# Performance work log

Measured on AMD Instinct MI355X. Metric: run time of the kernel, lower is better.

The kernel has to match this reference:

```python
import jax, jax.numpy as jnp
import numpy as np

N, E, H, ED = 100000, 1600000, 128, 64
BN_EPS = 1e-5


def setup_inputs() -> dict:
    key = jax.random.key(0)
    ks = jax.random.split(key, 8)
    s = 1.0 / np.sqrt(H)
    return {
        "h": jax.random.normal(ks[0], (N, H), jnp.float32),
        "ei": jax.random.randint(ks[1], (2, E), 0, N, jnp.int64),
        "ea": jax.random.normal(ks[2], (E, ED), jnp.float32),
        "valid_f": jnp.ones((N, 1), jnp.float32),
        "W_edge": jax.random.normal(ks[3], (ED, H), jnp.float32) / np.sqrt(ED),
        "b_edge": jnp.zeros((H,), jnp.float32),
        "W1": jax.random.normal(ks[4], (H, H), jnp.float32) * s,
        "b1": jnp.zeros((H,), jnp.float32),
        "W2": jax.random.normal(ks[5], (H, H), jnp.float32) * s,
        "b2": jnp.zeros((H,), jnp.float32),
        "eps_gine": jnp.zeros((1,), jnp.float32),
        "bn_gamma": jnp.ones((H,), jnp.float32),
        "bn_beta": jnp.zeros((H,), jnp.float32),
    }


def reference(h, ei, ea, valid_f, W_edge, b_edge, W1, b1, W2, b2, eps_gine, bn_gamma, bn_beta):
    src, dst = ei[0], ei[1]  # message flows j(src) -> i(dst)
    # GINE message: relu(x_j + lin(edge_attr))
    msg = jax.nn.relu(h[src] + ea @ W_edge + b_edge)          # [E, H]
    agg = jax.ops.segment_sum(msg, dst, num_segments=N)       # [N, H]
    # GIN update: mlp((1 + eps) * x_i + aggr)
    z = (1.0 + eps_gine[0]) * h + agg
    z = jax.nn.relu(z @ W1 + b1) @ W2 + b2                    # 2-layer MLP
    z = jax.nn.relu(z)
    # BatchNorm over nodes (training-mode batch stats, biased var)
    mean = jnp.mean(z, axis=0)
    var = jnp.var(z, axis=0)
    h_new = (z - mean) * jax.lax.rsqrt(var + BN_EPS) * bn_gamma + bn_beta
    # dropout p=0.0 -> identity; residual + valid mask
    return (h + h_new) * valid_f
```

## Files before the change

### kernel.cpp

```cpp
#include <hip/hip_runtime.h>

#define H 128
#define ED 64
#define CH 16
#define SCB 256
#define SCT 256

typedef __attribute__((ext_vector_type(8))) short short8;
typedef __attribute__((ext_vector_type(4))) float f32x4;
typedef __attribute__((ext_vector_type(4))) unsigned int u32x4;

__device__ __align__(16) float g_stats[256];

__device__ __forceinline__ unsigned short f2bf(float f) {
    unsigned u = __float_as_uint(f);
    unsigned r = u + 0x7fffu + ((u >> 16) & 1u);
    return (unsigned short)(r >> 16);
}
__device__ __forceinline__ float bf2f(unsigned short h) {
    return __uint_as_float(((unsigned)h) << 16);
}
__device__ __forceinline__ float4 ntld4(const float* p) {
    f32x4 v = __builtin_nontemporal_load((const f32x4*)p);
    return make_float4(v[0], v[1], v[2], v[3]);
}
__device__ __forceinline__ uint4 ntldu4(const unsigned* p) {
    u32x4 v = __builtin_nontemporal_load((const u32x4*)p);
    return make_uint4(v[0], v[1], v[2], v[3]);
}

__global__ void k_zero_stats() {
    if (threadIdx.x < 256) g_stats[threadIdx.x] = 0.f;
}

__global__ void k_hist(const int* __restrict__ ei, int* __restrict__ cnt, int E) {
    if (blockIdx.x == 0 && threadIdx.x < 256) g_stats[threadIdx.x] = 0.f;
    for (int e = blockIdx.x * blockDim.x + threadIdx.x; e < E;
         e += gridDim.x * blockDim.x)
        atomicAdd(&cnt[ei[E + e]], 1);
}

__global__ __launch_bounds__(SCT) void k_scanA(const int* __restrict__ cnt,
                                               int* __restrict__ bsum, int N) {
    __shared__ int part[SCT];
    const int b = blockIdx.x, t = threadIdx.x;
    const int chunk = (N + SCB - 1) / SCB;
    const int tch = (chunk + SCT - 1) / SCT;
    const int lo = b * chunk + t * tch;
    const int hi = min(lo + tch, min((b + 1) * chunk, N));
    int s = 0;
    for (int i = lo; i < hi; ++i) s += (cnt[i] + 15) >> 4;
    part[t] = s;
    __syncthreads();
    for (int d = SCT / 2; d > 0; d >>= 1) {
        if (t < d) part[t] += part[t + d];
        __syncthreads();
    }
    if (t == 0) bsum[b] = part[0];
}

__global__ __launch_bounds__(SCB) void k_scanB(const int* __restrict__ bsum,
                                               int* __restrict__ bpre,
                                               int* __restrict__ toffN) {
    __shared__ int part[SCB];
    const int t = threadIdx.x;
    int v = bsum[t];
    part[t] = v;
    __syncthreads();
    for (int d = 1; d < SCB; d <<= 1) {
        int x = (t >= d) ? part[t - d] : 0;
        __syncthreads();
        part[t] += x;
        __syncthreads();
    }
    bpre[t] = part[t] - v;
    if (t == SCB - 1) *toffN = part[t];
}

__global__ __launch_bounds__(SCT) void k_scanC(const int* __restrict__ cnt,
                                               const int* __restrict__ bpre,
                                               int* __restrict__ toff,
                                               int* __restrict__ tileDst, int N) {
    __shared__ int part[SCT];
    const int b = blockIdx.x, t = threadIdx.x;
    const int chunk = (N + SCB - 1) / SCB;
    const int tch = (chunk + SCT - 1) / SCT;
    const int lo = b * chunk + t * tch;
    const int hi = min(lo + tch, min((b + 1) * chunk, N));
    int ls = 0;
    for (int i = lo; i < hi; ++i) ls += (cnt[i] + 15) >> 4;
    part[t] = ls;
    __syncthreads();
    for (int d = 1; d < SCT; d <<= 1) {
        int x = (t >= d) ? part[t - d] : 0;
        __syncthreads();
        part[t] += x;
        __syncthreads();
    }
    int run = bpre[b] + part[t] - ls;
    for (int i = lo; i < hi; ++i) {
        toff[i] = run;
        int c = (cnt[i] + 15) >> 4;
        for (int j = 0; j < c; ++j) tileDst[run + j] = i;
        run += c;
    }
}

__global__ void k_fillp(const int* __restrict__ ei, const int* __restrict__ toff,
                        int* __restrict__ cur, int* __restrict__ tilePerm, int E) {
    for (int e = blockIdx.x * blockDim.x + threadIdx.x; e < E;
         e += gridDim.x * blockDim.x) {
        int d = ei[E + e];
        int pos = atomicAdd(&cur[d], 1);
        int tile = toff[d] + (pos >> 4);
        tilePerm[(tile << 4) + (pos & 15)] = e;
    }
}

__global__ __launch_bounds__(256, 3) void k_edge_t(
    const float* __restrict__ hN, const int* __restrict__ ei,
    const float* __restrict__ ea, const float* __restrict__ We,
    const float* __restrict__ be, const int* __restrict__ toff,
    const int* __restrict__ tileDst, const int* __restrict__ tilePerm,
    float* __restrict__ agg, int N, int E)
{
    __shared__ __align__(16) short sBf[8][2][64][8];
    const int tid = threadIdx.x;
    for (int idx = tid; idx < 8 * 2 * 64; idx += 256) {
        int t = idx >> 7, s = (idx >> 6) & 1, ll = idx & 63;
        int ra = ll & 15, kgg = ll >> 4;
        short8 f;
#pragma unroll
        for (int b = 0; b < 8; ++b) {
            int k = (s << 5) + (kgg << 3) + b;
            f[b] = (short)f2bf(We[k * H + (t << 4) + ra]);
        }
        *(short8*)&sBf[t][s][ll][0] = f;
    }
    const int l = tid & 63, w = tid >> 6;
    const int rA = l & 15, kg = l >> 4;
    float beT[8];
#pragma unroll
    for (int t = 0; t < 8; ++t) beT[t] = be[(t << 4) + rA];
    __syncthreads();

    const int nT = toff[N];
    const int gw = (blockIdx.x << 2) | w;
    const int nW = gridDim.x << 2;
    if (gw >= nT) return;

    int peC, srcC, dstC;
    float4 ea0, ea1, ea2, ea3;
    int peN;
    {
        peC = tilePerm[(gw << 4) + rA];
        dstC = tileDst[gw];
        srcC = (peC >= 0) ? ei[peC] : -1;
        const float* ar = ea + (size_t)max(peC, 0) * ED + (kg << 3);
        ea0 = ntld4(ar);      ea1 = ntld4(ar + 4);
        ea2 = ntld4(ar + 32); ea3 = ntld4(ar + 36);
        peN = (gw + nW < nT) ? tilePerm[((gw + nW) << 4) + rA] : -1;
    }

    for (int tt = gw; tt < nT; tt += nW) {
        const int s0 = __shfl(srcC, (kg << 2) + 0);
        const int s1 = __shfl(srcC, (kg << 2) + 1);
        const int s2 = __shfl(srcC, (kg << 2) + 2);
        const int s3 = __shfl(srcC, (kg << 2) + 3);
        float hv0[8], hv1[8], hv2[8], hv3[8];
        {
            const float* hp0 = hN + (size_t)max(s0, 0) * H + rA;
            const float* hp1 = hN + (size_t)max(s1, 0) * H + rA;
            const float* hp2 = hN + (size_t)max(s2, 0) * H + rA;
            const float* hp3 = hN + (size_t)max(s3, 0) * H + rA;
#pragma unroll
            for (int t = 0; t < 8; ++t) {
                hv0[t] = hp0[t << 4]; hv1[t] = hp1[t << 4];
                hv2[t] = hp2[t << 4]; hv3[t] = hp3[t << 4];
            }
        }
        const int ttN = tt + nW;
        int srcN = -1, dstN = 0;
        float4 eb0, eb1, eb2, eb3;
        eb0 = eb1 = eb2 = eb3 = make_float4(0.f, 0.f, 0.f, 0.f);
        if (ttN < nT) {
            srcN = (peN >= 0) ? ei[peN] : -1;
            dstN = tileDst[ttN];
            const float* ar = ea + (size_t)max(peN, 0) * ED + (kg << 3);
            eb0 = ntld4(ar);      eb1 = ntld4(ar + 4);
            eb2 = ntld4(ar + 32); eb3 = ntld4(ar + 36);
        }
        const int ttF = tt + 2 * nW;
        const int peF = (ttF < nT) ? tilePerm[(ttF << 4) + rA] : -1;

        short8 A0, A1;
        A0[0] = f2bf(ea0.x); A0[1] = f2bf(ea0.y); A0[2] = f2bf(ea0.z); A0[3] = f2bf(ea0.w);
        A0[4] = f2bf(ea1.x); A0[5] = f2bf(ea1.y); A0[6] = f2bf(ea1.z); A0[7] = f2bf(ea1.w);
        A1[0] = f2bf(ea2.x); A1[1] = f2bf(ea2.y); A1[2] = f2bf(ea2.z); A1[3] = f2bf(ea2.w);
        A1[4] = f2bf(ea3.x); A1[5] = f2bf(ea3.y); A1[6] = f2bf(ea3.z); A1[7] = f2bf(ea3.w);
        f32x4 C[8];
#pragma unroll
        for (int t = 0; t < 8; ++t) {
            short8 b0 = *(const short8*)&sBf[t][0][l][0];
            short8 b1 = *(const short8*)&sBf[t][1][l][0];
            f32x4 c = __builtin_amdgcn_mfma_f32_16x16x32_bf16(
                A0, b0, (f32x4){0.f, 0.f, 0.f, 0.f}, 0, 0, 0);
            C[t] = __builtin_amdgcn_mfma_f32_16x16x32_bf16(A1, b1, c, 0, 0, 0);
        }

        const float ok0 = (s0 >= 0) ? 1.f : 0.f;
        const float ok1 = (s1 >= 0) ? 1.f : 0.f;
        const float ok2 = (s2 >= 0) ? 1.f : 0.f;
        const float ok3 = (s3 >= 0) ? 1.f : 0.f;
        float pacc[8];
#pragma unroll
        for (int t = 0; t < 8; ++t) {
            float v = fmaxf(C[t][0] + hv0[t] + beT[t], 0.f) * ok0
                    + fmaxf(C[t][1] + hv1[t] + beT[t], 0.f) * ok1
                    + fmaxf(C[t][2] + hv2[t] + beT[t], 0.f) * ok2
                    + fmaxf(C[t][3] + hv3[t] + beT[t], 0.f) * ok3;
            v += __shfl_xor(v, 16);
            v += __shfl_xor(v, 32);
            pacc[t] = v;
        }
        float vlo = (kg == 0) ? pacc[0] : (kg == 1) ? pacc[1] : (kg == 2) ? pacc[2] : pacc[3];
        float vhi = (kg == 0) ? pacc[4] : (kg == 1) ? pacc[5] : (kg == 2) ? pacc[6] : pacc[7];
        float* qp = agg + (size_t)dstC * H + l;
        atomicAdd(qp, vlo);
        atomicAdd(qp + 64, vhi);

        peC = peN; srcC = srcN; dstC = dstN;
        ea0 = eb0; ea1 = eb1; ea2 = eb2; ea3 = eb3;
        peN = peF;
    }
}

__global__ __launch_bounds__(256, 2) void k_mlp1(
    const float* __restrict__ hN, float* zb, const float* __restrict__ W1,
    const float* __restrict__ b1, const float* __restrict__ epsp, int N)
{
    __shared__ __align__(16) short sBf[8][4][64][8];
    const int tid = threadIdx.x;
    for (int idx = tid; idx < 8 * 4 * 64; idx += 256) {
        int t = idx >> 8, s = (idx >> 6) & 3, ll = idx & 63;
        int ra = ll & 15, kgg = ll >> 4;
        short8 f;
#pragma unroll
        for (int b = 0; b < 8; ++b) {
            int k = (s << 5) + (kgg << 3) + b;
            f[b] = (short)f2bf(W1[k * H + (t << 4) + ra]);
        }
        *(short8*)&sBf[t][s][ll][0] = f;
    }
    __syncthreads();
    const int l = tid & 63, w = tid >> 6;
    const int rA = l & 15, kg = l >> 4;
    const float e1 = 1.f + epsp[0];
    float bT[8];
#pragma unroll
    for (int t = 0; t < 8; ++t) bT[t] = b1[(t << 4) + rA];

    const int nT = (N + CH - 1) / CH;
    for (int tt = blockIdx.x * 4 + w; tt < nT; tt += gridDim.x * 4) {
        const int n0 = tt << 4;
        const int row = min(n0 + rA, N - 1);
        const float* hrow = hN + (size_t)row * H;
        const float* arow = (const float*)zb + (size_t)row * H;
        f32x4 C[8];
#pragma unroll
        for (int t = 0; t < 8; ++t) C[t] = (f32x4){0.f, 0.f, 0.f, 0.f};

        const float* hp = hrow + (kg << 3);
        const float* ap = arow + (kg << 3);
        float4 h0 = ntld4(hp), h1 = ntld4(hp + 4);
        float4 g0 = ntld4(ap), g1 = ntld4(ap + 4);
#pragma unroll
        for (int s = 0; s < 4; ++s) {
            float4 h0n, h1n, g0n, g1n;
            if (s < 3) {
                const float* hp2 = hrow + ((s + 1) << 5) + (kg << 3);
                const float* ap2 = arow + ((s + 1) << 5) + (kg << 3);
                h0n = ntld4(hp2); h1n = ntld4(hp2 + 4);
                g0n = ntld4(ap2); g1n = ntld4(ap2 + 4);
            }
            float z[8];
            z[0] = fmaf(e1, h0.x, g0.x); z[1] = fmaf(e1, h0.y, g0.y);
            z[2] = fmaf(e1, h0.z, g0.z); z[3] = fmaf(e1, h0.w, g0.w);
            z[4] = fmaf(e1, h1.x, g1.x); z[5] = fmaf(e1, h1.y, g1.y);
            z[6] = fmaf(e1, h1.z, g1.z); z[7] = fmaf(e1, h1.w, g1.w);
            short8 ah, al;
#pragma unroll
            for (int j = 0; j < 8; ++j) {
                unsigned short hi = f2bf(z[j]);
                ah[j] = (short)hi;
                al[j] = (short)f2bf(z[j] - bf2f(hi));
            }
#pragma unroll
            for (int t = 0; t < 8; ++t) {
                short8 B = *(const short8*)&sBf[t][s][l][0];
                C[t] = __builtin_amdgcn_mfma_f32_16x16x32_bf16(ah, B, C[t], 0, 0, 0);
                C[t] = __builtin_amdgcn_mfma_f32_16x16x32_bf16(al, B, C[t], 0, 0, 0);
            }
            if (s < 3) { h0 = h0n; h1 = h1n; g0 = g0n; g1 = g1n; }
        }
#pragma unroll
        for (int t = 0; t < 8; ++t) {
#pragma unroll
            for (int rg = 0; rg < 4; ++rg) {
                int n = n0 + (kg << 2) + rg;
                float y = fmaxf(C[t][rg] + bT[t], 0.f);
                unsigned short hi = f2bf(y);
                unsigned short lo = f2bf(y - bf2f(hi));
                if (n < N)
                    ((unsigned*)zb)[(size_t)n * H + (t << 4) + rA] =
                        ((unsigned)hi << 16) | (unsigned)lo;
            }
        }
    }
}

__global__ __launch_bounds__(256, 2) void k_mlp2(
    float* zb, const float* __restrict__ W2, const float* __restrict__ b2, int N)
{
    __shared__ __align__(16) short sBf[8][4][64][8];
    const int tid = threadIdx.x;
    for (int idx = tid; idx < 8 * 4 * 64; idx += 256) {
        int t = idx >> 8, s = (idx >> 6) & 3, ll = idx & 63;
        int ra = ll & 15, kgg = ll >> 4;
        short8 f;
#pragma unroll
        for (int b = 0; b < 8; ++b) {
            int k = (s << 5) + (kgg << 3) + b;
            f[b] = (short)f2bf(W2[k * H + (t << 4) + ra]);
        }
        *(short8*)&sBf[t][s][ll][0] = f;
    }
    __syncthreads();
    const int l = tid & 63, w = tid >> 6;
    const int rA = l & 15, kg = l >> 4;
    float bT[8];
#pragma unroll
    for (int t = 0; t < 8; ++t) bT[t] = b2[(t << 4) + rA];
    float ps[8], pq[8];
#pragma unroll
    for (int t = 0; t < 8; ++t) { ps[t] = 0.f; pq[t] = 0.f; }

    const int nT = (N + CH - 1) / CH;
    for (int tt = blockIdx.x * 4 + w; tt < nT; tt += gridDim.x * 4) {
        const int n0 = tt << 4;
        const int row = min(n0 + rA, N - 1);
        const unsigned* yrow = (const unsigned*)zb + (size_t)row * H;
        f32x4 C[8];
#pragma unroll
        for (int t = 0; t < 8; ++t) C[t] = (f32x4){0.f, 0.f, 0.f, 0.f};

        const unsigned* yp = yrow + (kg << 3);
        uint4 u0 = ntldu4(yp), u1 = ntldu4(yp + 4);
#pragma unroll
        for (int s = 0; s < 4; ++s) {
            uint4 u0n, u1n;
            if (s < 3) {
                const unsigned* yp2 = yrow + ((s + 1) << 5) + (kg << 3);
                u0n = ntldu4(yp2); u1n = ntldu4(yp2 + 4);
            }
            short8 ah, al;
            ah[0] = (short)(u0.x >> 16); al[0] = (short)(u0.x & 0xffffu);
            ah[1] = (short)(u0.y >> 16); al[1] = (short)(u0.y & 0xffffu);
            ah[2] = (short)(u0.z >> 16); al[2] = (short)(u0.z & 0xffffu);
            ah[3] = (short)(u0.w >> 16); al[3] = (short)(u0.w & 0xffffu);
            ah[4] = (short)(u1.x >> 16); al[4] = (short)(u1.x & 0xffffu);
            ah[5] = (short)(u1.y >> 16); al[5] = (short)(u1.y & 0xffffu);
            ah[6] = (short)(u1.z >> 16); al[6] = (short)(u1.z & 0xffffu);
            ah[7] = (short)(u1.w >> 16); al[7] = (short)(u1.w & 0xffffu);
#pragma unroll
            for (int t = 0; t < 8; ++t) {
                short8 B = *(const short8*)&sBf[t][s][l][0];
                C[t] = __builtin_amdgcn_mfma_f32_16x16x32_bf16(ah, B, C[t], 0, 0, 0);
                C[t] = __builtin_amdgcn_mfma_f32_16x16x32_bf16(al, B, C[t], 0, 0, 0);
            }
            if (s < 3) { u0 = u0n; u1 = u1n; }
        }
#pragma unroll
        for (int t = 0; t < 8; ++t) {
#pragma unroll
            for (int rg = 0; rg < 4; ++rg) {
                int n = n0 + (kg << 2) + rg;
                float z2 = fmaxf(C[t][rg] + bT[t], 0.f);
                bool v = (n < N);
                if (v) ((float*)zb)[(size_t)n * H + (t << 4) + rA] = z2;
                float zc = v ? z2 : 0.f;
                ps[t] += zc;
                pq[t] += zc * zc;
            }
        }
    }
#pragma unroll
    for (int t = 0; t < 8; ++t) {
        float a = ps[t]; a += __shfl_xor(a, 16); a += __shfl_xor(a, 32); ps[t] = a;
        float b = pq[t]; b += __shfl_xor(b, 16); b += __shfl_xor(b, 32); pq[t] = b;
    }
    if (l < 16) {
#pragma unroll
        for (int t = 0; t < 8; ++t) {
            atomicAdd(&g_stats[(t << 4) + l], ps[t]);
            atomicAdd(&g_stats[128 + (t << 4) + l], pq[t]);
        }
    }
}

__global__ void k_final(const float* __restrict__ hN, const float* __restrict__ valid,
                        const float* __restrict__ gamma, const float* __restrict__ beta,
                        float invN, float* __restrict__ out, int N)
{
    __shared__ float sSc[H], sSh[H];
    if (threadIdx.x < H) {
        int t = threadIdx.x;
        float mean = g_stats[t] * invN;
        float var  = g_stats[H + t] * invN - mean * mean;
        float sc = gamma[t] * rsqrtf(var + 1e-5f);
        sSc[t] = sc;
        sSh[t] = beta[t] - mean * sc;
    }
    __syncthreads();
    const int total = N * (H / 4);
    for (int i = blockIdx.x * blockDim.x + threadIdx.x; i < total;
         i += gridDim.x * blockDim.x) {
        int col4 = i & 31;
        int n = i >> 5;
        float4 z = ((float4*)out)[i];
        float4 hv = ntld4(hN + (size_t)i * 4);
        float4 sc = *(const float4*)&sSc[col4 * 4];
        float4 sh = *(const float4*)&sSh[col4 * 4];
        float vf = valid[n];
        float4 r;
        r.x = (hv.x + fmaf(z.x, sc.x, sh.x)) * vf;
        r.y = (hv.y + fmaf(z.y, sc.y, sh.y)) * vf;
        r.z = (hv.z + fmaf(z.z, sc.z, sh.z)) * vf;
        r.w = (hv.w + fmaf(z.w, sc.w, sh.w)) * vf;
        ((float4*)out)[i] = r;
    }
}

__global__ __launch_bounds__(512, 4) void k_edge_a(
    const float* __restrict__ hN, const int* __restrict__ ei,
    const float* __restrict__ ea, const float* __restrict__ We,
    const float* __restrict__ be, float* __restrict__ agg, int E)
{
    __shared__ __align__(16) short sBf[8][2][64][8];
    const int tid = threadIdx.x;
    for (int idx = tid; idx < 8 * 2 * 64; idx += 512) {
        int t = idx >> 7, s = (idx >> 6) & 1, ll = idx & 63;
        int ra = ll & 15, kgg = ll >> 4;
        short8 f;
#pragma unroll
        for (int b = 0; b < 8; ++b) {
            int k = (s << 5) + (kgg << 3) + b;
            f[b] = (short)f2bf(We[k * H + (t << 4) + ra]);
        }
        *(short8*)&sBf[t][s][ll][0] = f;
    }
    const int l = tid & 63, w = tid >> 6;
    const int rA = l & 15, kg = l >> 4;
    float beT[8];
#pragma unroll
    for (int t = 0; t < 8; ++t) beT[t] = be[(t << 4) + rA];
    __syncthreads();

    const int nT = (E + CH - 1) / CH;
    for (int tt = (blockIdx.x << 3) | w; tt < nT; tt += gridDim.x << 3) {
        int e0 = tt * CH;
        const float* ar = ea + (size_t)min(e0 + rA, E - 1) * ED + (kg << 3);
        float4 a0 = *(const float4*)ar,        a1 = *(const float4*)(ar + 4);
        float4 a2 = *(const float4*)(ar + 32), a3 = *(const float4*)(ar + 36);
        int r0 = min(e0 + (kg << 2) + 0, E - 1), r1 = min(e0 + (kg << 2) + 1, E - 1);
        int r2 = min(e0 + (kg << 2) + 2, E - 1), r3 = min(e0 + (kg << 2) + 3, E - 1);
        int s0 = ei[r0], s1 = ei[r1], s2 = ei[r2], s3 = ei[r3];
        int d0 = ei[E + r0], d1 = ei[E + r1], d2 = ei[E + r2], d3 = ei[E + r3];
        float hv0[8], hv1[8], hv2[8], hv3[8];
        const float* hp0 = hN + (size_t)s0 * H + rA;
        const float* hp1 = hN + (size_t)s1 * H + rA;
        const float* hp2 = hN + (size_t)s2 * H + rA;
        const float* hp3 = hN + (size_t)s3 * H + rA;
#pragma unroll
        for (int t = 0; t < 8; ++t) {
            hv0[t] = hp0[t << 4]; hv1[t] = hp1[t << 4];
            hv2[t] = hp2[t << 4]; hv3[t] = hp3[t << 4];
        }
        short8 A0, A1;
        A0[0] = f2bf(a0.x); A0[1] = f2bf(a0.y); A0[2] = f2bf(a0.z); A0[3] = f2bf(a0.w);
        A0[4] = f2bf(a1.x); A0[5] = f2bf(a1.y); A0[6] = f2bf(a1.z); A0[7] = f2bf(a1.w);
        A1[0] = f2bf(a2.x); A1[1] = f2bf(a2.y); A1[2] = f2bf(a2.z); A1[3] = f2bf(a2.w);
        A1[4] = f2bf(a3.x); A1[5] = f2bf(a3.y); A1[6] = f2bf(a3.z); A1[7] = f2bf(a3.w);
        f32x4 C[8];
#pragma unroll
        for (int t = 0; t < 8; ++t) {
            short8 b0 = *(const short8*)&sBf[t][0][l][0];
            short8 b1 = *(const short8*)&sBf[t][1][l][0];
            f32x4 c = __builtin_amdgcn_mfma_f32_16x16x32_bf16(
                A0, b0, (f32x4){0.f, 0.f, 0.f, 0.f}, 0, 0, 0);
            C[t] = __builtin_amdgcn_mfma_f32_16x16x32_bf16(A1, b1, c, 0, 0, 0);
        }
        const int m = E - e0;
        const int r = kg << 2;
        const bool ok0 = (r + 0) < m, ok1 = (r + 1) < m;
        const bool ok2 = (r + 2) < m, ok3 = (r + 3) < m;
        float* q0 = agg + (size_t)d0 * H + rA;
        float* q1 = agg + (size_t)d1 * H + rA;
        float* q2 = agg + (size_t)d2 * H + rA;
        float* q3 = agg + (size_t)d3 * H + rA;
#pragma unroll
        for (int t = 0; t < 8; ++t) {
            if (ok0) atomicAdd(q0 + (t << 4), fmaxf(C[t][0] + hv0[t] + beT[t], 0.f));
            if (ok1) atomicAdd(q1 + (t << 4), fmaxf(C[t][1] + hv1[t] + beT[t], 0.f));
            if (ok2) atomicAdd(q2 + (t << 4), fmaxf(C[t][2] + hv2[t] + beT[t], 0.f));
            if (ok3) atomicAdd(q3 + (t << 4), fmaxf(C[t][3] + hv3[t] + beT[t], 0.f));
        }
    }
}

extern "C" void kernel_launch(void* const* d_in, const int* in_sizes, int n_in,
                              void* d_out, int out_size, void* d_ws, size_t ws_size,
                              hipStream_t stream) {
    const float* hN    = (const float*)d_in[0];
    const int*   ei    = (const int*)d_in[1];
    const float* ea    = (const float*)d_in[2];
    const float* valid = (const float*)d_in[3];
    const float* We    = (const float*)d_in[4];
    const float* be    = (const float*)d_in[5];
    const float* W1    = (const float*)d_in[6];
    const float* b1    = (const float*)d_in[7];
    const float* W2    = (const float*)d_in[8];
    const float* b2    = (const float*)d_in[9];
    const float* epsg  = (const float*)d_in[10];
    const float* gamma = (const float*)d_in[11];
    const float* beta  = (const float*)d_in[12];
    float* out = (float*)d_out;

    const int N = in_sizes[0] / H;
    const int E = in_sizes[1] / 2;

    const int Tcap = (E + 15) / 16 + N;
    const size_t need = ((size_t)3 * N + 1 + 2 * SCB + (size_t)17 * Tcap) * sizeof(int);

    (void)hipMemsetAsync(d_out, 0, (size_t)out_size * sizeof(float), stream);

    if (ws_size >= need) {
        int* cnt      = (int*)d_ws;
        int* cur      = cnt + N;
        int* toff     = cur + N;
        int* bsum     = toff + N + 1;
        int* bpre     = bsum + SCB;
        int* tileDst  = bpre + SCB;
        int* tilePerm = tileDst + Tcap;

        (void)hipMemsetAsync(cnt, 0, (size_t)2 * N * sizeof(int), stream);
        (void)hipMemsetAsync(tilePerm, 0xFF, (size_t)16 * Tcap * sizeof(int), stream);
        k_hist<<<2048, 256, 0, stream>>>(ei, cnt, E);
        k_scanA<<<SCB, SCT, 0, stream>>>(cnt, bsum, N);
        k_scanB<<<1, SCB, 0, stream>>>(bsum, bpre, toff + N);
        k_scanC<<<SCB, SCT, 0, stream>>>(cnt, bpre, toff, tileDst, N);
        k_fillp<<<2048, 256, 0, stream>>>(ei, toff, cur, tilePerm, E);
        k_edge_t<<<2048, 256, 0, stream>>>(hN, ei, ea, We, be, toff, tileDst,
                                           tilePerm, out, N, E);
    } else {
        k_zero_stats<<<1, 256, 0, stream>>>();
        k_edge_a<<<1024, 512, 0, stream>>>(hN, ei, ea, We, be, out, E);
    }

    k_mlp1<<<512, 256, 0, stream>>>(hN, out, W1, b1, epsg, N);
    k_mlp2<<<512, 256, 0, stream>>>(out, W2, b2, N);
    k_final<<<2048, 256, 0, stream>>>(hN, valid, gamma, beta, 1.0f / (float)N,
                                      out, N);
}
```

Measured before the change: 606.9 us.

## Replace three-pass tile scan with atomic tile allocation and fuse MLP layers

Replaces the three scan kernels with a single kernel that hands out tile ranges per destination node using a global atomic counter, and pads only the last tile of each node instead of memsetting the whole tilePerm buffer. The two MLP kernels are fused into one: the first layer's split-bf16 output is staged in per-wave LDS instead of round-tripping through global memory, and both weight matrices are held in shared memory. This removes kernel launches, a large memset and the intermediate global traffic. In exchange, tile order becomes nondeterministic, which loses destination locality, and the larger LDS footprint and 512-thread blocks may reduce occupancy.

```diff
diff --git a/kernel.cpp b/kernel.cpp
--- a/kernel.cpp
+++ b/kernel.cpp
@@ -3,8 +3,6 @@
 #define H 128
 #define ED 64
 #define CH 16
-#define SCB 256
-#define SCT 256
 
 typedef __attribute__((ext_vector_type(8))) short short8;
 typedef __attribute__((ext_vector_type(4))) float f32x4;
@@ -23,10 +21,6 @@
 __device__ __forceinline__ float4 ntld4(const float* p) {
     f32x4 v = __builtin_nontemporal_load((const f32x4*)p);
     return make_float4(v[0], v[1], v[2], v[3]);
-}
-__device__ __forceinline__ uint4 ntldu4(const unsigned* p) {
-    u32x4 v = __builtin_nontemporal_load((const u32x4*)p);
-    return make_uint4(v[0], v[1], v[2], v[3]);
 }
 
 __global__ void k_zero_stats() {
@@ -40,69 +34,22 @@
         atomicAdd(&cnt[ei[E + e]], 1);
 }
 
-__global__ __launch_bounds__(SCT) void k_scanA(const int* __restrict__ cnt,
-                                               int* __restrict__ bsum, int N) {
-    __shared__ int part[SCT];
-    const int b = blockIdx.x, t = threadIdx.x;
-    const int chunk = (N + SCB - 1) / SCB;
-    const int tch = (chunk + SCT - 1) / SCT;
-    const int lo = b * chunk + t * tch;
-    const int hi = min(lo + tch, min((b + 1) * chunk, N));
-    int s = 0;
-    for (int i = lo; i < hi; ++i) s += (cnt[i] + 15) >> 4;
-    part[t] = s;
-    __syncthreads();
-    for (int d = SCT / 2; d > 0; d >>= 1) {
-        if (t < d) part[t] += part[t + d];
-        __syncthreads();
-    }
-    if (t == 0) bsum[b] = part[0];
-}
-
-__global__ __launch_bounds__(SCB) void k_scanB(const int* __restrict__ bsum,
-                                               int* __restrict__ bpre,
-                                               int* __restrict__ toffN) {
-    __shared__ int part[SCB];
-    const int t = threadIdx.x;
-    int v = bsum[t];
-    part[t] = v;
-    __syncthreads();
-    for (int d = 1; d < SCB; d <<= 1) {
-        int x = (t >= d) ? part[t - d] : 0;
-        __syncthreads();
-        part[t] += x;
-        __syncthreads();
-    }
-    bpre[t] = part[t] - v;
-    if (t == SCB - 1) *toffN = part[t];
-}
-
-__global__ __launch_bounds__(SCT) void k_scanC(const int* __restrict__ cnt,
-                                               const int* __restrict__ bpre,
-                                               int* __restrict__ toff,
-                                               int* __restrict__ tileDst, int N) {
-    __shared__ int part[SCT];
-    const int b = blockIdx.x, t = threadIdx.x;
-    const int chunk = (N + SCB - 1) / SCB;
-    const int tch = (chunk + SCT - 1) / SCT;
-    const int lo = b * chunk + t * tch;
-    const int hi = min(lo + tch, min((b + 1) * chunk, N));
-    int ls = 0;
-    for (int i = lo; i < hi; ++i) ls += (cnt[i] + 15) >> 4;
-    part[t] = ls;
-    __syncthreads();
-    for (int d = 1; d < SCT; d <<= 1) {
-        int x = (t >= d) ? part[t - d] : 0;
-        __syncthreads();
-        part[t] += x;
-        __syncthreads();
-    }
-    int run = bpre[b] + part[t] - ls;
-    for (int i = lo; i < hi; ++i) {
-        toff[i] = run;
-        int c = (cnt[i] + 15) >> 4;
-        for (int j = 0; j < c; ++j) tileDst[run + j] = i;
-        run += c;
+__global__ void k_tiles(const int* __restrict__ cnt, int* __restrict__ toff,
+                        int* __restrict__ tileDst, int* __restrict__ tilePerm,
+                        int* __restrict__ tcnt, int N) {
+    for (int d = blockIdx.x * blockDim.x + threadIdx.x; d < N;
+         d += gridDim.x * blockDim.x) {
+        int c = cnt[d];
+        int nt = (c + 15) >> 4;
+        if (nt == 0) continue;
+        int base = atomicAdd(tcnt, nt);
+        toff[d] = base;
+        for (int j = 0; j < nt; ++j) tileDst[base + j] = d;
+        int pad = c & 15;
+        if (pad) {
+            int* lastp = tilePerm + ((size_t)(base + nt - 1) << 4);
+            for (int j = pad; j < 16; ++j) lastp[j] = -1;
+        }
     }
 }
 
@@ -113,14 +60,14 @@
         int d = ei[E + e];
         int pos = atomicAdd(&cur[d], 1);
         int tile = toff[d] + (pos >> 4);
-        tilePerm[(tile << 4) + (pos & 15)] = e;
+        tilePerm[((size_t)tile << 4) + (pos & 15)] = e;
     }
 }
 
 __global__ __launch_bounds__(256, 3) void k_edge_t(
     const float* __restrict__ hN, const int* __restrict__ ei,
     const float* __restrict__ ea, const float* __restrict__ We,
-    const float* __restrict__ be, const int* __restrict__ toff,
+    const float* __restrict__ be, const int* __restrict__ tcnt,
     const int* __restrict__ tileDst, const int* __restrict__ tilePerm,
     float* __restrict__ agg, int N, int E)
 {
@@ -144,7 +91,7 @@
     for (int t = 0; t < 8; ++t) beT[t] = be[(t << 4) + rA];
     __syncthreads();
 
-    const int nT = toff[N];
+    const int nT = tcnt[0];
     const int gw = (blockIdx.x << 2) | w;
     const int nW = gridDim.x << 2;
     if (gw >= nT) return;
@@ -153,13 +100,13 @@
     float4 ea0, ea1, ea2, ea3;
     int peN;
     {
-        peC = tilePerm[(gw << 4) + rA];
+        peC = tilePerm[((size_t)gw << 4) + rA];
         dstC = tileDst[gw];
         srcC = (peC >= 0) ? ei[peC] : -1;
         const float* ar = ea + (size_t)max(peC, 0) * ED + (kg << 3);
         ea0 = ntld4(ar);      ea1 = ntld4(ar + 4);
         ea2 = ntld4(ar + 32); ea3 = ntld4(ar + 36);
-        peN = (gw + nW < nT) ? tilePerm[((gw + nW) << 4) + rA] : -1;
+        peN = (gw + nW < nT) ? tilePerm[((size_t)(gw + nW) << 4) + rA] : -1;
     }
 
     for (int tt = gw; tt < nT; tt += nW) {
@@ -191,7 +138,7 @@
             eb2 = ntld4(ar + 32); eb3 = ntld4(ar + 36);
         }
         const int ttF = tt + 2 * nW;
-        const int peF = (ttF < nT) ? tilePerm[(ttF << 4) + rA] : -1;
+        const int peF = (ttF < nT) ? tilePerm[((size_t)ttF << 4) + rA] : -1;
 
         short8 A0, A1;
         A0[0] = f2bf(ea0.x); A0[1] = f2bf(ea0.y); A0[2] = f2bf(ea0.z); A0[3] = f2bf(ea0.w);
@@ -235,33 +182,45 @@
     }
 }
 
-__global__ __launch_bounds__(256, 2) void k_mlp1(
-    const float* __restrict__ hN, float* zb, const float* __restrict__ W1,
-    const float* __restrict__ b1, const float* __restrict__ epsp, int N)
+__global__ __launch_bounds__(512, 2) void k_mlp(
+    const float* __restrict__ hN, float* zb,
+    const float* __restrict__ W1, const float* __restrict__ b1,
+    const float* __restrict__ W2, const float* __restrict__ b2,
+    const float* __restrict__ epsp, int N)
 {
-    __shared__ __align__(16) short sBf[8][4][64][8];
+    __shared__ __align__(16) short sB1[8][4][64][8];
+    __shared__ __align__(16) short sB2[8][4][64][8];
+    __shared__ __align__(16) unsigned sY[8][16][132];
     const int tid = threadIdx.x;
-    for (int idx = tid; idx < 8 * 4 * 64; idx += 256) {
+    for (int idx = tid; idx < 8 * 4 * 64; idx += 512) {
         int t = idx >> 8, s = (idx >> 6) & 3, ll = idx & 63;
         int ra = ll & 15, kgg = ll >> 4;
-        short8 f;
+        short8 f1, f2;
 #pragma unroll
         for (int b = 0; b < 8; ++b) {
             int k = (s << 5) + (kgg << 3) + b;
-            f[b] = (short)f2bf(W1[k * H + (t << 4) + ra]);
-        }
-        *(short8*)&sBf[t][s][ll][0] = f;
+            f1[b] = (short)f2bf(W1[k * H + (t << 4) + ra]);
+            f2[b] = (short)f2bf(W2[k * H + (t << 4) + ra]);
+        }
+        *(short8*)&sB1[t][s][ll][0] = f1;
+        *(short8*)&sB2[t][s][ll][0] = f2;
     }
     __syncthreads();
     const int l = tid & 63, w = tid >> 6;
     const int rA = l & 15, kg = l >> 4;
     const float e1 = 1.f + epsp[0];
-    float bT[8];
-#pragma unroll
-    for (int t = 0; t < 8; ++t) bT[t] = b1[(t << 4) + rA];
+    float bT1[8], bT2[8];
+#pragma unroll
+    for (int t = 0; t < 8; ++t) {
+        bT1[t] = b1[(t << 4) + rA];
+        bT2[t] = b2[(t << 4) + rA];
+    }
+    float ps[8], pq[8];
+#pragma unroll
+    for (int t = 0; t < 8; ++t) { ps[t] = 0.f; pq[t] = 0.f; }
 
     const int nT = (N + CH - 1) / CH;
-    for (int tt = blockIdx.x * 4 + w; tt < nT; tt += gridDim.x * 4) {
+    for (int tt = blockIdx.x * 8 + w; tt < nT; tt += gridDim.x * 8) {
         const int n0 = tt << 4;
         const int row = min(n0 + rA, N - 1);
         const float* hrow = hN + (size_t)row * H;
@@ -270,19 +229,12 @@
 #pragma unroll
         for (int t = 0; t < 8; ++t) C[t] = (f32x4){0.f, 0.f, 0.f, 0.f};
 
-        const float* hp = hrow + (kg << 3);
-        const float* ap = arow + (kg << 3);
-        float4 h0 = ntld4(hp), h1 = ntld4(hp + 4);
-        float4 g0 = ntld4(ap), g1 = ntld4(ap + 4);
 #pragma unroll
         for (int s = 0; s < 4; ++s) {
-            float4 h0n, h1n, g0n, g1n;
-            if (s < 3) {
-                const float* hp2 = hrow + ((s + 1) << 5) + (kg << 3);
-                const float* ap2 = arow + ((s + 1) << 5) + (kg << 3);
-                h0n = ntld4(hp2); h1n = ntld4(hp2 + 4);
-                g0n = ntld4(ap2); g1n = ntld4(ap2 + 4);
-            }
+            const float* hp = hrow + (s << 5) + (kg << 3);
+            const float* ap = arow + (s << 5) + (kg << 3);
+            float4 h0 = ntld4(hp), h1 = ntld4(hp + 4);
+            float4 g0 = ntld4(ap), g1 = ntld4(ap + 4);
             float z[8];
             z[0] = fmaf(e1, h0.x, g0.x); z[1] = fmaf(e1, h0.y, g0.y);
             z[2] = fmaf(e1, h0.z, g0.z); z[3] = fmaf(e1, h0.w, g0.w);
@@ -297,72 +249,31 @@
             }
 #pragma unroll
             for (int t = 0; t < 8; ++t) {
-                short8 B = *(const short8*)&sBf[t][s][l][0];
+                short8 B = *(const short8*)&sB1[t][s][l][0];
                 C[t] = __builtin_amdgcn_mfma_f32_16x16x32_bf16(ah, B, C[t], 0, 0, 0);
                 C[t] = __builtin_amdgcn_mfma_f32_16x16x32_bf16(al, B, C[t], 0, 0, 0);
             }
-            if (s < 3) { h0 = h0n; h1 = h1n; g0 = g0n; g1 = g1n; }
         }
 #pragma unroll
         for (int t = 0; t < 8; ++t) {
 #pragma unroll
             for (int rg = 0; rg < 4; ++rg) {
-                int n = n0 + (kg << 2) + rg;
-                float y = fmaxf(C[t][rg] + bT[t], 0.f);
+                float y = fmaxf(C[t][rg] + bT1[t], 0.f);
                 unsigned short hi = f2bf(y);
                 unsigned short lo = f2bf(y - bf2f(hi));
-                if (n < N)
-                    ((unsigned*)zb)[(size_t)n * H + (t << 4) + rA] =
-                        ((unsigned)hi << 16) | (unsigned)lo;
-            }
-        }
-    }
-}
-
-__global__ __launch_bounds__(256, 2) void k_mlp2(
-    float* zb, const float* __restrict__ W2, const float* __restrict__ b2, int N)
-{
-    __shared__ __align__(16) short sBf[8][4][64][8];
-    const int tid = threadIdx.x;
-    for (int idx = tid; idx < 8 * 4 * 64; idx += 256) {
-        int t = idx >> 8, s = (idx >> 6) & 3, ll = idx & 63;
-        int ra = ll & 15, kgg = ll >> 4;
-        short8 f;
-#pragma unroll
-        for (int b = 0; b < 8; ++b) {
-            int k = (s << 5) + (kgg << 3) + b;
-            f[b] = (short)f2bf(W2[k * H + (t << 4) + ra]);
-        }
-        *(short8*)&sBf[t][s][ll][0] = f;
-    }
-    __syncthreads();
-    const int l = tid & 63, w = tid >> 6;
-    const int rA = l & 15, kg = l >> 4;
-    float bT[8];
-#pragma unroll
-    for (int t = 0; t < 8; ++t) bT[t] = b2[(t << 4) + rA];
-    float ps[8], pq[8];
-#pragma unroll
-    for (int t = 0; t < 8; ++t) { ps[t] = 0.f; pq[t] = 0.f; }
-
-    const int nT = (N + CH - 1) / CH;
-    for (int tt = blockIdx.x * 4 + w; tt < nT; tt += gridDim.x * 4) {
-        const int n0 = tt << 4;
-        const int row = min(n0 + rA, N - 1);
-        const unsigned* yrow = (const unsigned*)zb + (size_t)row * H;
-        f32x4 C[8];
+                sY[w][(kg << 2) + rg][(t << 4) + rA] =
+                    ((unsigned)hi << 16) | (unsigned)lo;
+            }
+        }
+        __builtin_amdgcn_wave_barrier();
+
 #pragma unroll
         for (int t = 0; t < 8; ++t) C[t] = (f32x4){0.f, 0.f, 0.f, 0.f};
-
-        const unsigned* yp = yrow + (kg << 3);
-        uint4 u0 = ntldu4(yp), u1 = ntldu4(yp + 4);
 #pragma unroll
         for (int s = 0; s < 4; ++s) {
-            uint4 u0n, u1n;
-            if (s < 3) {
-                const unsigned* yp2 = yrow + ((s + 1) << 5) + (kg << 3);
-                u0n = ntldu4(yp2); u1n = ntldu4(yp2 + 4);
-            }
+            const unsigned* yp = &sY[w][rA][(s << 5) + (kg << 3)];
+            uint4 u0 = *(const uint4*)yp;
+            uint4 u1 = *(const uint4*)(yp + 4);
             short8 ah, al;
             ah[0] = (short)(u0.x >> 16); al[0] = (short)(u0.x & 0xffffu);
             ah[1] = (short)(u0.y >> 16); al[1] = (short)(u0.y & 0xffffu);
@@ -374,18 +285,17 @@
             ah[7] = (short)(u1.w >> 16); al[7] = (short)(u1.w & 0xffffu);
 #pragma unroll
             for (int t = 0; t < 8; ++t) {
-                short8 B = *(const short8*)&sBf[t][s][l][0];
+                short8 B = *(const short8*)&sB2[t][s][l][0];
                 C[t] = __builtin_amdgcn_mfma_f32_16x16x32_bf16(ah, B, C[t], 0, 0, 0);
                 C[t] = __builtin_amdgcn_mfma_f32_16x16x32_bf16(al, B, C[t], 0, 0, 0);
             }
-            if (s < 3) { u0 = u0n; u1 = u1n; }
         }
 #pragma unroll
         for (int t = 0; t < 8; ++t) {
 #pragma unroll
             for (int rg = 0; rg < 4; ++rg) {
                 int n = n0 + (kg << 2) + rg;
-                float z2 = fmaxf(C[t][rg] + bT[t], 0.f);
+                float z2 = fmaxf(C[t][rg] + bT2[t], 0.f);
                 bool v = (n < N);
                 if (v) ((float*)zb)[(size_t)n * H + (t << 4) + rA] = z2;
                 float zc = v ? z2 : 0.f;
@@ -393,6 +303,7 @@
                 pq[t] += zc * zc;
             }
         }
+        __builtin_amdgcn_wave_barrier();
     }
 #pragma unroll
     for (int t = 0; t < 8; ++t) {
@@ -540,35 +451,30 @@
     const int E = in_sizes[1] / 2;
 
     const int Tcap = (E + 15) / 16 + N;
-    const size_t need = ((size_t)3 * N + 1 + 2 * SCB + (size_t)17 * Tcap) * sizeof(int);
+    const size_t need = ((size_t)3 * N + 1 + (size_t)17 * Tcap) * sizeof(int);
 
     (void)hipMemsetAsync(d_out, 0, (size_t)out_size * sizeof(float), stream);
 
     if (ws_size >= need) {
         int* cnt      = (int*)d_ws;
         int* cur      = cnt + N;
-        int* toff     = cur + N;
-        int* bsum     = toff + N + 1;
-        int* bpre     = bsum + SCB;
-        int* tileDst  = bpre + SCB;
+        int* tcnt     = cur + N;
+        int* toff     = tcnt + 1;
+        int* tileDst  = toff + N;
         int* tilePerm = tileDst + Tcap;
 
-        (void)hipMemsetAsync(cnt, 0, (size_t)2 * N * sizeof(int), stream);
-        (void)hipMemsetAsync(tilePerm, 0xFF, (size_t)16 * Tcap * sizeof(int), stream);
+        (void)hipMemsetAsync(cnt, 0, ((size_t)2 * N + 1) * sizeof(int), stream);
         k_hist<<<2048, 256, 0, stream>>>(ei, cnt, E);
-        k_scanA<<<SCB, SCT, 0, stream>>>(cnt, bsum, N);
-        k_scanB<<<1, SCB, 0, stream>>>(bsum, bpre, toff + N);
-        k_scanC<<<SCB, SCT, 0, stream>>>(cnt, bpre, toff, tileDst, N);
+        k_tiles<<<512, 256, 0, stream>>>(cnt, toff, tileDst, tilePerm, tcnt, N);
         k_fillp<<<2048, 256, 0, stream>>>(ei, toff, cur, tilePerm, E);
-        k_edge_t<<<2048, 256, 0, stream>>>(hN, ei, ea, We, be, toff, tileDst,
+        k_edge_t<<<2048, 256, 0, stream>>>(hN, ei, ea, We, be, tcnt, tileDst,
                                            tilePerm, out, N, E);
     } else {
         k_zero_stats<<<1, 256, 0, stream>>>();
         k_edge_a<<<1024, 512, 0, stream>>>(hN, ei, ea, We, be, out, E);
     }
 
-    k_mlp1<<<512, 256, 0, stream>>>(hN, out, W1, b1, epsg, N);
-    k_mlp2<<<512, 256, 0, stream>>>(out, W2, b2, N);
+    k_mlp<<<256, 512, 0, stream>>>(hN, out, W1, b1, W2, b2, epsg, N);
     k_final<<<2048, 256, 0, stream>>>(hN, valid, gamma, beta, 1.0f / (float)N,
                                       out, N);
 }
```

After: 619.4 us. +2.1%, slower.
